# Kernel optimization log

Measured on AMD Instinct MI355X. Metric: run time of the kernel, lower is better.

The kernel has to match this reference:

```python
import jax, jax.numpy as jnp
import numpy as np

B, L, C = 8, 8192, 256
FOCAL_LEVEL = 3
KERNELS = [3, 5, 7]  # focal_factor*k + focal_x[0]
LN_EPS = 1e-3  # keras LayerNormalization default epsilon


def _gelu(x):
    return jax.nn.gelu(x, approximate=False)  # keras 'gelu' is exact


def _layernorm(x, g, b):
    m = jnp.mean(x, axis=-1, keepdims=True)
    v = jnp.var(x, axis=-1, keepdims=True)
    return (x - m) * jax.lax.rsqrt(v + LN_EPS) * g + b


def _conv1d_same(x, w, b):
    # x: [B,L,Cin], w: [K,Cin,Cout]
    y = jax.lax.conv_general_dilated(x, w, window_strides=(1,), padding='SAME',
                                     dimension_numbers=('NWC', 'WIO', 'NWC'))
    return y + b


def setup_inputs() -> dict:
    key = jax.random.key(0)
    ks = jax.random.split(key, 16)
    s = 0.02
    inp = {
        'x': jax.random.normal(ks[0], (B, L, C), dtype=jnp.float32),
        'f_w': jax.random.normal(ks[1], (C, 2 * C + FOCAL_LEVEL + 1), dtype=jnp.float32) * s,
        'f_b': jnp.zeros((2 * C + FOCAL_LEVEL + 1,), dtype=jnp.float32),
        'h_w': jax.random.normal(ks[2], (1, C, C), dtype=jnp.float32) * s,
        'h_b': jnp.zeros((C,), dtype=jnp.float32),
        'proj_w': jax.random.normal(ks[3], (C, C), dtype=jnp.float32) * s,
        'proj_b': jnp.zeros((C,), dtype=jnp.float32),
    }
    for l, K in enumerate(KERNELS):
        inp[f'conv_w{l}'] = jax.random.normal(ks[4 + l], (K, C, C), dtype=jnp.float32) * s
        inp[f'conv_b{l}'] = jnp.zeros((C,), dtype=jnp.float32)
        inp[f'ln_g{l}'] = jnp.ones((C,), dtype=jnp.float32)
        inp[f'ln_b{l}'] = jnp.zeros((C,), dtype=jnp.float32)
    return inp


def reference(x, f_w, f_b,
              conv_w0, conv_b0, ln_g0, ln_b0,
              conv_w1, conv_b1, ln_g1, ln_b1,
              conv_w2, conv_b2, ln_g2, ln_b2,
              h_w, h_b, proj_w, proj_b):
    x_fea = x @ f_w + f_b                      # [B,L,2C+4]
    q = x_fea[..., :C]
    ctx = x_fea[..., C:2 * C]
    gates = x_fea[..., 2 * C:]                 # [B,L,4]

    levels = [(conv_w0, conv_b0, ln_g0, ln_b0),
              (conv_w1, conv_b1, ln_g1, ln_b1),
              (conv_w2, conv_b2, ln_g2, ln_b2)]

    ctx_all = jnp.zeros_like(ctx)
    for l, (cw, cb, lg, lb) in enumerate(levels):
        ctx = _layernorm(_gelu(_conv1d_same(ctx, cw, cb)), lg, lb)
        ctx_all = ctx_all + ctx * gates[..., l:l + 1]

    # global average pool gate (broadcasts over L)
    ctx_global = jnp.mean(ctx, axis=1, keepdims=True) * gates[..., FOCAL_LEVEL:]
    ctx_all = ctx_all + ctx_global

    # h: 1x1 conv == dense
    ctx_all = jnp.einsum('blc,cd->bld', ctx_all, h_w[0]) + h_b
    x_out = (q * ctx_all) @ proj_w + proj_b    # proj_drop is identity at inference
    return x_out
```

## Files before the change

### kernel.cpp

```cpp
#include <hip/hip_runtime.h>
#include <math.h>

#define CDIM 256
#define LSEQ 8192
#define BATCH 8
#define MTOT (BATCH * LSEQ)
#define PADROWS 8208
#define PAD0 8

typedef unsigned short ushort_t;
typedef unsigned int uint_t;

typedef __bf16 bf16x8 __attribute__((ext_vector_type(8)));
typedef float f32x4 __attribute__((ext_vector_type(4)));

__device__ __forceinline__ ushort_t f2bf(float f) {
    union { float f; uint_t u; } v; v.f = f;
    uint_t u = v.u;
    return (ushort_t)((u + 0x7FFFu + ((u >> 16) & 1u)) >> 16);
}
__device__ __forceinline__ float bf2f(ushort_t h) {
    union { uint_t u; float f; } v; v.u = ((uint_t)h) << 16;
    return v.f;
}
__device__ __forceinline__ float gelu_exact(float x) {
    return 0.5f * x * (1.0f + erff(x * 0.70710678118654752440f));
}

__device__ __forceinline__ void gload16(const ushort_t* g, ushort_t* lds) {
    __builtin_amdgcn_global_load_lds(
        reinterpret_cast<__attribute__((address_space(1))) uint_t*>(
            reinterpret_cast<uintptr_t>(g)),
        reinterpret_cast<__attribute__((address_space(3))) uint_t*>(
            reinterpret_cast<uintptr_t>(lds)),
        16, 0, 0);
}

__global__ __launch_bounds__(256) void cvt_gates(
    const float* __restrict__ x, const float* __restrict__ f_w,
    const float* __restrict__ f_b,
    ushort_t* __restrict__ x_bf, float* __restrict__ gates)
{
    __shared__ float fcol[256][4];
    int tid = threadIdx.x;
    #pragma unroll
    for (int j = 0; j < 4; ++j) fcol[tid][j] = f_w[(size_t)tid * 516 + 512 + j];
    __syncthreads();
    int w = tid >> 6, l = tid & 63;
    size_t t = (size_t)blockIdx.x * 4 + w;
    float4 xv = ((const float4*)(x + t * CDIM))[l];
    ((ushort4*)(x_bf + t * CDIM))[l] =
        make_ushort4(f2bf(xv.x), f2bf(xv.y), f2bf(xv.z), f2bf(xv.w));
    int c = l * 4;
    float a[4];
    #pragma unroll
    for (int j = 0; j < 4; ++j)
        a[j] = xv.x * fcol[c][j] + xv.y * fcol[c + 1][j] + xv.z * fcol[c + 2][j] + xv.w * fcol[c + 3][j];
    #pragma unroll
    for (int off = 32; off >= 1; off >>= 1)
        #pragma unroll
        for (int j = 0; j < 4; ++j) a[j] += __shfl_xor(a[j], off);
    if (l == 0) {
        #pragma unroll
        for (int j = 0; j < 4; ++j) gates[t * 4 + j] = a[j] + f_b[512 + j];
    }
}

__global__ __launch_bounds__(256) void prep_weights(
    const float* __restrict__ f_w,  const float* __restrict__ c0,
    const float* __restrict__ c1,   const float* __restrict__ c2,
    const float* __restrict__ h_w,  const float* __restrict__ p_w,
    ushort_t* __restrict__ f_wT, ushort_t* __restrict__ c0T,
    ushort_t* __restrict__ c1T,  ushort_t* __restrict__ c2T,
    ushort_t* __restrict__ h_wT, ushort_t* __restrict__ p_wT)
{
    __shared__ float t[32][33];
    int r = blockIdx.x;
    const float* in; ushort_t* out; int Kt, ldin;
    if (r < 128)              { in = f_w; out = f_wT; Kt = 8;  ldin = 516; }
    else if ((r -= 128) < 192){ in = c0;  out = c0T;  Kt = 24; ldin = 256; }
    else if ((r -= 192) < 320){ in = c1;  out = c1T;  Kt = 40; ldin = 256; }
    else if ((r -= 320) < 448){ in = c2;  out = c2T;  Kt = 56; ldin = 256; }
    else if ((r -= 448) < 64) { in = h_w; out = h_wT; Kt = 8;  ldin = 256; }
    else                      { r -= 64; in = p_w; out = p_wT; Kt = 8; ldin = 256; }
    int K = Kt * 32;
    int k0 = (r % Kt) * 32, n0 = (r / Kt) * 32;
    int tx = threadIdx.x & 31, ty = threadIdx.x >> 5;
    #pragma unroll
    for (int i = 0; i < 4; i++) {
        int k = k0 + ty + i * 8;
        t[ty + i * 8][tx] = in[(size_t)k * ldin + n0 + tx];
    }
    __syncthreads();
    #pragma unroll
    for (int i = 0; i < 4; i++) {
        int n = n0 + ty + i * 8;
        out[(size_t)n * K + k0 + tx] = f2bf(t[tx][ty + i * 8]);
    }
}

__global__ __launch_bounds__(256) void zero_guards_all(ushort_t* __restrict__ ctx_base) {
    int i = blockIdx.x * 256 + threadIdx.x;
    int buf = i >> 15;
    int j = i & 32767;
    int c = j & 255;
    int rr = (j >> 8) & 15;
    int b = j >> 12;
    size_t row = (size_t)b * PADROWS + ((rr < 8) ? rr : (PADROWS - 16 + rr));
    ctx_base[((size_t)buf * BATCH * PADROWS + row) * CDIM + c] = 0;
}

__global__ __launch_bounds__(256) void fea_gemm(
    const ushort_t* __restrict__ A, const ushort_t* __restrict__ BT,
    const float* __restrict__ bias,
    ushort_t* __restrict__ q_out, ushort_t* __restrict__ ctx_pad)
{
    __shared__ __align__(16) ushort_t As[128 * 32];
    __shared__ __align__(16) ushort_t Bs[128 * 32];
    int tid = threadIdx.x;
    int w = tid >> 6, l = tid & 63;
    int bn = blockIdx.x * 128;
    int by = blockIdx.y;
    long arow0 = (long)by * 128;
    int crow0 = by * 128;

    int wr = w >> 1, wc = w & 1;
    int lr = l & 15, lk = (l >> 4) * 8;
    int sr = l >> 2;
    int sc = (l & 3) * 8;

    f32x4 acc[4][4] = {};

    for (int kt = 0; kt < 8; ++kt) {
        int k0 = kt << 5;
        #pragma unroll
        for (int jj = 0; jj < 2; ++jj) {
            int j = w * 2 + jj;
            int r = j * 16 + sr;
            gload16(A + (arow0 + r) * CDIM + (k0 + sc), &As[j * 512]);
            gload16(BT + (long)(bn + r) * 256 + (k0 + sc), &Bs[j * 512]);
        }
        __syncthreads();
        bf16x8 av[4], bv[4];
        #pragma unroll
        for (int m = 0; m < 4; ++m)
            av[m] = *reinterpret_cast<const bf16x8*>(&As[(wr * 64 + m * 16 + lr) * 32 + lk]);
        #pragma unroll
        for (int n = 0; n < 4; ++n)
            bv[n] = *reinterpret_cast<const bf16x8*>(&Bs[(wc * 64 + n * 16 + lr) * 32 + lk]);
        #pragma unroll
        for (int m = 0; m < 4; ++m)
            #pragma unroll
            for (int n = 0; n < 4; ++n)
                acc[m][n] = __builtin_amdgcn_mfma_f32_16x16x32_bf16(av[m], bv[n], acc[m][n], 0, 0, 0);
        __syncthreads();
    }

    int rbase = (l >> 4) * 4;
    #pragma unroll
    for (int n = 0; n < 4; ++n) {
        int col = bn + wc * 64 + n * 16 + lr;
        float bia = bias[col];
        #pragma unroll
        for (int m = 0; m < 4; ++m) {
            int rowb = crow0 + wr * 64 + m * 16 + rbase;
            #pragma unroll
            for (int r = 0; r < 4; ++r) {
                float v = acc[m][n][r] + bia;
                int row = rowb + r;
                if (col < CDIM) {
                    q_out[(size_t)row * CDIM + col] = f2bf(v);
                } else {
                    int bb = row >> 13, tb = row & (LSEQ - 1);
                    ctx_pad[((size_t)bb * PADROWS + PAD0 + tb) * CDIM + (col - CDIM)] = f2bf(v);
                }
            }
        }
    }
}

__device__ __forceinline__ void stageA128(const ushort_t* Arow0, int cc,
                                          ushort_t* asb, int tid, int w) {
    int row = tid >> 2, cp = tid & 3;
    int cg = cp ^ ((row >> 1) & 3);
    gload16(Arow0 + (size_t)row * CDIM + cc * 32 + cg * 8, asb + (size_t)(w * 64) * 8);
    if (tid < 64) {
        int o2 = 512 + tid;
        int row2 = o2 >> 2, cp2 = o2 & 3;
        int cg2 = cp2 ^ ((row2 >> 1) & 3);
        gload16(Arow0 + (size_t)row2 * CDIM + cc * 32 + cg2 * 8, asb + (size_t)512 * 8);
    }
}
__device__ __forceinline__ void stageB128(const ushort_t* BT, int Ktot, int koffB,
                                          ushort_t* bsb, int tid) {
    #pragma unroll
    for (int i = 0; i < 2; ++i) {
        int o = tid + i * 512;
        int n = o >> 2, cp = o & 3;
        int cg = cp ^ ((n >> 1) & 3);
        gload16(BT + (size_t)n * Ktot + koffB + cg * 8,
                bsb + (size_t)((o >> 6) * 64) * 8);
    }
}

__global__ __launch_bounds__(512, 4) void conv_fused(
    const ushort_t* __restrict__ A, const ushort_t* __restrict__ BT,
    const float* __restrict__ bias,
    const float* __restrict__ lng, const float* __restrict__ lnb,
    ushort_t* __restrict__ ctx_out, int KW, int Ktot)
{
    __shared__ __align__(16) ushort_t As2[2][144 * 32];
    __shared__ __align__(16) ushort_t Bs[2][256 * 32];

    int tid = threadIdx.x;
    int w = tid >> 6, l = tid & 63;
    int by = blockIdx.x;
    int b = by >> 6;
    int tloc = (by & 63) << 7;
    const ushort_t* Arow0 = A + ((size_t)b * PADROWS + PAD0 + tloc - 8) * CDIM;

    int wr = w >> 2;
    int wc = w & 3;
    int lr = l & 15;
    int quad = l >> 4;

    int P = KW >> 1;
    int hoff = 8 - P;
    f32x4 acc[4][4] = {};

    stageA128(Arow0, 0, As2[0], tid, w);
    stageB128(BT, Ktot, 0, Bs[0], tid);
    __syncthreads();

    int nIt = KW * 8;
    int it = 0;
    for (int c = 0; c < 8; ++c) {
        for (int tap = 0; tap < KW; ++tap, ++it) {
            if (tap == 0 && c < 7)
                stageA128(Arow0, c + 1, As2[(c + 1) & 1], tid, w);
            if (it + 1 < nIt) {
                int tapn = tap + 1, cn = c;
                if (tapn == KW) { tapn = 0; cn = c + 1; }
                stageB128(BT, Ktot, tapn * 256 + cn * 32, Bs[(it + 1) & 1], tid);
            }
            const ushort_t* asb = As2[c & 1];
            const ushort_t* bsb = Bs[it & 1];
            bf16x8 av[4], bv[4];
            #pragma unroll
            for (int m = 0; m < 4; ++m) {
                int row = wr * 64 + m * 16 + lr + tap + hoff;
                int cs = quad ^ ((row >> 1) & 3);
                av[m] = *reinterpret_cast<const bf16x8*>(&asb[row * 32 + cs * 8]);
            }
            #pragma unroll
            for (int n = 0; n < 4; ++n) {
                int nn = wc * 64 + n * 16 + lr;
                int cs = quad ^ ((nn >> 1) & 3);
                bv[n] = *reinterpret_cast<const bf16x8*>(&bsb[nn * 32 + cs * 8]);
            }
            #pragma unroll
            for (int m = 0; m < 4; ++m)
                #pragma unroll
                for (int n = 0; n < 4; ++n)
                    acc[m][n] = __builtin_amdgcn_mfma_f32_16x16x32_bf16(av[m], bv[n], acc[m][n], 0, 0, 0);
            __syncthreads();
        }
    }

    float* rs = (float*)&Bs[0][0];
    float* rq = rs + 512;
    float bias_c[4], lng_c[4], lnb_c[4];
    #pragma unroll
    for (int n = 0; n < 4; ++n) {
        int col = wc * 64 + n * 16 + lr;
        bias_c[n] = bias[col];
        lng_c[n] = lng[col];
        lnb_c[n] = lnb[col];
    }
    #pragma unroll
    for (int m = 0; m < 4; ++m) {
        #pragma unroll
        for (int r = 0; r < 4; ++r) {
            float s = 0.0f, sq = 0.0f;
            #pragma unroll
            for (int n = 0; n < 4; ++n) {
                float v = acc[m][n][r] + bias_c[n];
                v = gelu_exact(v);
                acc[m][n][r] = v;
                s += v; sq += v * v;
            }
            s += __shfl_xor(s, 1);  sq += __shfl_xor(sq, 1);
            s += __shfl_xor(s, 2);  sq += __shfl_xor(sq, 2);
            s += __shfl_xor(s, 4);  sq += __shfl_xor(sq, 4);
            s += __shfl_xor(s, 8);  sq += __shfl_xor(sq, 8);
            if (lr == 0) {
                int rl = wr * 64 + m * 16 + quad * 4 + r;
                rs[rl * 4 + wc] = s;
                rq[rl * 4 + wc] = sq;
            }
        }
    }
    __syncthreads();
    #pragma unroll
    for (int m = 0; m < 4; ++m) {
        #pragma unroll
        for (int r = 0; r < 4; ++r) {
            int rl = wr * 64 + m * 16 + quad * 4 + r;
            float mean = (rs[rl * 4] + rs[rl * 4 + 1] + rs[rl * 4 + 2] + rs[rl * 4 + 3]) * (1.0f / 256.0f);
            float var = (rq[rl * 4] + rq[rl * 4 + 1] + rq[rl * 4 + 2] + rq[rl * 4 + 3]) * (1.0f / 256.0f) - mean * mean;
            float inv = rsqrtf(var + 1e-3f);
            int trow = tloc + rl;
            ushort_t* cp = ctx_out + ((size_t)b * PADROWS + PAD0 + trow) * CDIM;
            #pragma unroll
            for (int n = 0; n < 4; ++n) {
                int col = wc * 64 + n * 16 + lr;
                float y = (acc[m][n][r] - mean) * inv * lng_c[n] + lnb_c[n];
                cp[col] = f2bf(y);
            }
        }
    }
}

__global__ __launch_bounds__(256) void col_mean_partial(const ushort_t* __restrict__ ctx_pad,
                                                        float* __restrict__ partial) {
    int b = blockIdx.x, chunk = blockIdx.y, c = threadIdx.x;
    const ushort_t* base = ctx_pad + ((size_t)b * PADROWS + PAD0 + chunk * 256) * CDIM + c;
    float s = 0.0f;
    for (int r = 0; r < 256; ++r) s += bf2f(base[(size_t)r * CDIM]);
    partial[((size_t)b * 32 + chunk) * CDIM + c] = s;
}

__global__ __launch_bounds__(256) void col_mean_final(const float* __restrict__ partial,
                                                      float* __restrict__ meanv) {
    int b = blockIdx.x, c = threadIdx.x;
    float s = 0.0f;
    for (int i = 0; i < 32; ++i) s += partial[((size_t)b * 32 + i) * CDIM + c];
    meanv[b * CDIM + c] = s * (1.0f / (float)LSEQ);
}

__global__ __launch_bounds__(512) void tail_fused(
    const ushort_t* __restrict__ ctx0, const ushort_t* __restrict__ ctx1,
    const ushort_t* __restrict__ ctx2,
    const float* __restrict__ gates, const float* __restrict__ meanv,
    const ushort_t* __restrict__ q_bf,
    const ushort_t* __restrict__ h_wT, const float* __restrict__ h_b,
    const ushort_t* __restrict__ proj_wT, const float* __restrict__ proj_b,
    float* __restrict__ out)
{
    __shared__ __align__(16) char pool[81920];
    ushort_t* As1 = (ushort_t*)pool;
    ushort_t* Bs1 = (ushort_t*)(pool + 8192);
    ushort_t* QC  = (ushort_t*)pool;
    ushort_t* Bs2 = (ushort_t*)(pool + 65536);

    int tid = threadIdx.x;
    int w = tid >> 6, l = tid & 63;
    long grow0 = (long)blockIdx.x * 128;

    int wr = w >> 2;
    int wc = w & 3;
    int lr = l & 15;
    int quad = l >> 4;
    int lk = quad * 8;

    int arow = tid >> 2;
    int seg = tid & 3;
    long grow_st = grow0 + arow;
    int b_st = (int)(grow_st >> 13), tb_st = (int)(grow_st & (LSEQ - 1));
    size_t prow = ((size_t)b_st * PADROWS + PAD0 + tb_st) * CDIM;
    float4 gv = *(const float4*)(gates + grow_st * 4);

    f32x4 acc[4][4] = {};

    for (int kt = 0; kt < 8; ++kt) {
        int col = kt * 32 + seg * 8;
        ushort4 a0 = *(const ushort4*)(ctx0 + prow + col);
        ushort4 a1 = *(const ushort4*)(ctx0 + prow + col + 4);
        ushort4 b0 = *(const ushort4*)(ctx1 + prow + col);
        ushort4 b1 = *(const ushort4*)(ctx1 + prow + col + 4);
        ushort4 d0 = *(const ushort4*)(ctx2 + prow + col);
        ushort4 d1 = *(const ushort4*)(ctx2 + prow + col + 4);
        float4 m0 = *(const float4*)(meanv + b_st * CDIM + col);
        float4 m1 = *(const float4*)(meanv + b_st * CDIM + col + 4);
        ushort_t va[8] = { a0.x, a0.y, a0.z, a0.w, a1.x, a1.y, a1.z, a1.w };
        ushort_t vb[8] = { b0.x, b0.y, b0.z, b0.w, b1.x, b1.y, b1.z, b1.w };
        ushort_t vd[8] = { d0.x, d0.y, d0.z, d0.w, d1.x, d1.y, d1.z, d1.w };
        float mv[8] = { m0.x, m0.y, m0.z, m0.w, m1.x, m1.y, m1.z, m1.w };
        ushort_t ov[8];
        #pragma unroll
        for (int j = 0; j < 8; ++j)
            ov[j] = f2bf(bf2f(va[j]) * gv.x + bf2f(vb[j]) * gv.y +
                         bf2f(vd[j]) * gv.z + mv[j] * gv.w);
        *(ushort4*)(As1 + arow * 32 + seg * 8)     = make_ushort4(ov[0], ov[1], ov[2], ov[3]);
        *(ushort4*)(As1 + arow * 32 + seg * 8 + 4) = make_ushort4(ov[4], ov[5], ov[6], ov[7]);
        #pragma unroll
        for (int i = 0; i < 2; ++i) {
            int o = tid + i * 512;
            int n = o >> 2, cp = o & 3;
            gload16(h_wT + (size_t)n * 256 + kt * 32 + cp * 8,
                    Bs1 + (size_t)((o >> 6) * 64) * 8);
        }
        __syncthreads();
        bf16x8 av[4], bv[4];
        #pragma unroll
        for (int m = 0; m < 4; ++m)
            av[m] = *reinterpret_cast<const bf16x8*>(&As1[(wr * 64 + m * 16 + lr) * 32 + lk]);
        #pragma unroll
        for (int n = 0; n < 4; ++n)
            bv[n] = *reinterpret_cast<const bf16x8*>(&Bs1[(wc * 64 + n * 16 + lr) * 32 + lk]);
        #pragma unroll
        for (int m = 0; m < 4; ++m)
            #pragma unroll
            for (int n = 0; n < 4; ++n)
                acc[m][n] = __builtin_amdgcn_mfma_f32_16x16x32_bf16(av[m], bv[n], acc[m][n], 0, 0, 0);
        __syncthreads();
    }

    {
        float hb_c[4];
        #pragma unroll
        for (int n = 0; n < 4; ++n) hb_c[n] = h_b[wc * 64 + n * 16 + lr];
        #pragma unroll
        for (int m = 0; m < 4; ++m) {
            #pragma unroll
            for (int r = 0; r < 4; ++r) {
                int row = wr * 64 + m * 16 + quad * 4 + r;
                long grow = grow0 + row;
                #pragma unroll
                for (int n = 0; n < 4; ++n) {
                    int col = wc * 64 + n * 16 + lr;
                    float v = acc[m][n][r] + hb_c[n];
                    float qv = bf2f(q_bf[(size_t)grow * CDIM + col]);
                    int c16 = (col >> 3) ^ (row & 7);
                    QC[row * 256 + c16 * 8 + (col & 7)] = f2bf(qv * v);
                }
            }
        }
    }
    __syncthreads();

    f32x4 acc2[4][4] = {};
    for (int kt = 0; kt < 8; ++kt) {
        #pragma unroll
        for (int i = 0; i < 2; ++i) {
            int o = tid + i * 512;
            int n = o >> 2, cp = o & 3;
            gload16(proj_wT + (size_t)n * 256 + kt * 32 + cp * 8,
                    Bs2 + (size_t)((o >> 6) * 64) * 8);
        }
        __syncthreads();
        bf16x8 av[4], bv[4];
        #pragma unroll
        for (int m = 0; m < 4; ++m) {
            int row = wr * 64 + m * 16 + lr;
            int c16 = (kt * 4 + quad) ^ (row & 7);
            av[m] = *reinterpret_cast<const bf16x8*>(&QC[row * 256 + c16 * 8]);
        }
        #pragma unroll
        for (int n = 0; n < 4; ++n)
            bv[n] = *reinterpret_cast<const bf16x8*>(&Bs2[(wc * 64 + n * 16 + lr) * 32 + lk]);
        #pragma unroll
        for (int m = 0; m < 4; ++m)
            #pragma unroll
            for (int n = 0; n < 4; ++n)
                acc2[m][n] = __builtin_amdgcn_mfma_f32_16x16x32_bf16(av[m], bv[n], acc2[m][n], 0, 0, 0);
        __syncthreads();
    }

    int rbase = quad * 4;
    #pragma unroll
    for (int n = 0; n < 4; ++n) {
        int col = wc * 64 + n * 16 + lr;
        float pb = proj_b[col];
        #pragma unroll
        for (int m = 0; m < 4; ++m) {
            #pragma unroll
            for (int r = 0; r < 4; ++r) {
                long grow = grow0 + wr * 64 + m * 16 + rbase + r;
                out[(size_t)grow * CDIM + col] = acc2[m][n][r] + pb;
            }
        }
    }
}

extern "C" void kernel_launch(void* const* d_in, const int* in_sizes, int n_in,
                              void* d_out, int out_size, void* d_ws, size_t ws_size,
                              hipStream_t stream) {
    const float* x      = (const float*)d_in[0];
    const float* f_w    = (const float*)d_in[1];
    const float* f_b    = (const float*)d_in[2];
    const float* h_w    = (const float*)d_in[3];
    const float* h_b    = (const float*)d_in[4];
    const float* proj_w = (const float*)d_in[5];
    const float* proj_b = (const float*)d_in[6];
    const float* conv_w[3] = { (const float*)d_in[7],  (const float*)d_in[11], (const float*)d_in[15] };
    const float* conv_b[3] = { (const float*)d_in[8],  (const float*)d_in[12], (const float*)d_in[16] };
    const float* ln_g[3]   = { (const float*)d_in[9],  (const float*)d_in[13], (const float*)d_in[17] };
    const float* ln_b[3]   = { (const float*)d_in[10], (const float*)d_in[14], (const float*)d_in[18] };

    const size_t MC = (size_t)MTOT * CDIM;
    const size_t PADC = (size_t)BATCH * PADROWS * CDIM;
    char* w = (char*)d_ws;
    ushort_t* x_bf  = (ushort_t*)w;  w += MC * 2;
    ushort_t* q_bf  = (ushort_t*)w;  w += MC * 2;
    ushort_t* ctxF  = (ushort_t*)w;  w += PADC * 2;
    ushort_t* ctx0  = (ushort_t*)w;  w += PADC * 2;
    ushort_t* ctx1  = (ushort_t*)w;  w += PADC * 2;
    ushort_t* ctx2  = (ushort_t*)w;  w += PADC * 2;
    float* gates    = (float*)w;     w += (size_t)MTOT * 4 * 4;
    float* partial  = (float*)w;     w += (size_t)8 * 32 * CDIM * 4;
    float* meanv    = (float*)w;     w += (size_t)8 * CDIM * 4;
    ushort_t* f_wT  = (ushort_t*)w;  w += (size_t)512 * 256 * 2;
    ushort_t* convT0 = (ushort_t*)w; w += (size_t)768 * 256 * 2;
    ushort_t* convT1 = (ushort_t*)w; w += (size_t)1280 * 256 * 2;
    ushort_t* convT2 = (ushort_t*)w; w += (size_t)1792 * 256 * 2;
    ushort_t* h_wT   = (ushort_t*)w; w += (size_t)256 * 256 * 2;
    ushort_t* proj_wT = (ushort_t*)w; w += (size_t)256 * 256 * 2;

    dim3 blk(256);

    cvt_gates<<<dim3(MTOT / 4), blk, 0, stream>>>(x, f_w, f_b, x_bf, gates);
    prep_weights<<<dim3(1216), blk, 0, stream>>>(f_w, conv_w[0], conv_w[1], conv_w[2],
        h_w, proj_w, f_wT, convT0, convT1, convT2, h_wT, proj_wT);
    zero_guards_all<<<dim3(512), blk, 0, stream>>>(ctxF);

    fea_gemm<<<dim3(4, 512), blk, 0, stream>>>(x_bf, f_wT, f_b, q_bf, ctxF);

    conv_fused<<<dim3(512), dim3(512), 0, stream>>>(ctxF, convT0, conv_b[0],
        ln_g[0], ln_b[0], ctx0, 3, 768);
    conv_fused<<<dim3(512), dim3(512), 0, stream>>>(ctx0, convT1, conv_b[1],
        ln_g[1], ln_b[1], ctx1, 5, 1280);
    conv_fused<<<dim3(512), dim3(512), 0, stream>>>(ctx1, convT2, conv_b[2],
        ln_g[2], ln_b[2], ctx2, 7, 1792);

    col_mean_partial<<<dim3(BATCH, 32), blk, 0, stream>>>(ctx2, partial);
    col_mean_final<<<dim3(BATCH), blk, 0, stream>>>(partial, meanv);

    tail_fused<<<dim3(512), dim3(512), 0, stream>>>(ctx0, ctx1, ctx2,
        gates, meanv, q_bf, h_wT, h_b, proj_wT, proj_b, (float*)d_out);
}
```

Baseline: 388.8 us.

## Split fused tail into separate combine+h GEMM and proj GEMM kernels

Replaces the single fused tail kernel, which kept the q*ctx intermediate in 80KB of shared memory, with two kernels using 256 threads and 128x128 tiles tiled over N. The gated combine and h projection write q*ctx as bf16 to global memory, reusing the x_bf buffer, and a separate GEMM applies proj. This aims for better occupancy and a smaller LDS footprint. The cost is an extra global round trip of the intermediate and recomputing the gated combine for each N tile.

```diff
diff --git a/kernel.cpp b/kernel.cpp
--- a/kernel.cpp
+++ b/kernel.cpp
@@ -338,34 +338,27 @@
     meanv[b * CDIM + c] = s * (1.0f / (float)LSEQ);
 }
 
-__global__ __launch_bounds__(512) void tail_fused(
+__global__ __launch_bounds__(256) void combine_h_gemm(
     const ushort_t* __restrict__ ctx0, const ushort_t* __restrict__ ctx1,
     const ushort_t* __restrict__ ctx2,
     const float* __restrict__ gates, const float* __restrict__ meanv,
     const ushort_t* __restrict__ q_bf,
     const ushort_t* __restrict__ h_wT, const float* __restrict__ h_b,
-    const ushort_t* __restrict__ proj_wT, const float* __restrict__ proj_b,
-    float* __restrict__ out)
+    ushort_t* __restrict__ qc_out)
 {
-    __shared__ __align__(16) char pool[81920];
-    ushort_t* As1 = (ushort_t*)pool;
-    ushort_t* Bs1 = (ushort_t*)(pool + 8192);
-    ushort_t* QC  = (ushort_t*)pool;
-    ushort_t* Bs2 = (ushort_t*)(pool + 65536);
-
+    __shared__ __align__(16) ushort_t As[128 * 32];
+    __shared__ __align__(16) ushort_t Bs[128 * 32];
     int tid = threadIdx.x;
     int w = tid >> 6, l = tid & 63;
-    long grow0 = (long)blockIdx.x * 128;
-
-    int wr = w >> 2;
-    int wc = w & 3;
-    int lr = l & 15;
-    int quad = l >> 4;
-    int lk = quad * 8;
-
-    int arow = tid >> 2;
-    int seg = tid & 3;
-    long grow_st = grow0 + arow;
+    int bn = blockIdx.x * 128;
+    long arow0 = (long)blockIdx.y * 128;
+
+    int wr = w >> 1, wc = w & 1;
+    int lr = l & 15, lk = (l >> 4) * 8;
+
+    int arow = tid >> 1;
+    int seg = tid & 1;
+    long grow_st = arow0 + arow;
     int b_st = (int)(grow_st >> 13), tb_st = (int)(grow_st & (LSEQ - 1));
     size_t prow = ((size_t)b_st * PADROWS + PAD0 + tb_st) * CDIM;
     float4 gv = *(const float4*)(gates + grow_st * 4);
@@ -373,41 +366,50 @@
     f32x4 acc[4][4] = {};
 
     for (int kt = 0; kt < 8; ++kt) {
-        int col = kt * 32 + seg * 8;
-        ushort4 a0 = *(const ushort4*)(ctx0 + prow + col);
-        ushort4 a1 = *(const ushort4*)(ctx0 + prow + col + 4);
-        ushort4 b0 = *(const ushort4*)(ctx1 + prow + col);
-        ushort4 b1 = *(const ushort4*)(ctx1 + prow + col + 4);
-        ushort4 d0 = *(const ushort4*)(ctx2 + prow + col);
-        ushort4 d1 = *(const ushort4*)(ctx2 + prow + col + 4);
-        float4 m0 = *(const float4*)(meanv + b_st * CDIM + col);
-        float4 m1 = *(const float4*)(meanv + b_st * CDIM + col + 4);
-        ushort_t va[8] = { a0.x, a0.y, a0.z, a0.w, a1.x, a1.y, a1.z, a1.w };
-        ushort_t vb[8] = { b0.x, b0.y, b0.z, b0.w, b1.x, b1.y, b1.z, b1.w };
-        ushort_t vd[8] = { d0.x, d0.y, d0.z, d0.w, d1.x, d1.y, d1.z, d1.w };
-        float mv[8] = { m0.x, m0.y, m0.z, m0.w, m1.x, m1.y, m1.z, m1.w };
-        ushort_t ov[8];
-        #pragma unroll
-        for (int j = 0; j < 8; ++j)
-            ov[j] = f2bf(bf2f(va[j]) * gv.x + bf2f(vb[j]) * gv.y +
-                         bf2f(vd[j]) * gv.z + mv[j] * gv.w);
-        *(ushort4*)(As1 + arow * 32 + seg * 8)     = make_ushort4(ov[0], ov[1], ov[2], ov[3]);
-        *(ushort4*)(As1 + arow * 32 + seg * 8 + 4) = make_ushort4(ov[4], ov[5], ov[6], ov[7]);
+        int col = kt * 32 + seg * 16;
+        ushort4 c0a = *(const ushort4*)(ctx0 + prow + col);
+        ushort4 c0b = *(const ushort4*)(ctx0 + prow + col + 4);
+        ushort4 c0c = *(const ushort4*)(ctx0 + prow + col + 8);
+        ushort4 c0d = *(const ushort4*)(ctx0 + prow + col + 12);
+        ushort4 c1a = *(const ushort4*)(ctx1 + prow + col);
+        ushort4 c1b = *(const ushort4*)(ctx1 + prow + col + 4);
+        ushort4 c1c = *(const ushort4*)(ctx1 + prow + col + 8);
+        ushort4 c1d = *(const ushort4*)(ctx1 + prow + col + 12);
+        ushort4 c2a = *(const ushort4*)(ctx2 + prow + col);
+        ushort4 c2b = *(const ushort4*)(ctx2 + prow + col + 4);
+        ushort4 c2c = *(const ushort4*)(ctx2 + prow + col + 8);
+        ushort4 c2d = *(const ushort4*)(ctx2 + prow + col + 12);
+        const float* mv = meanv + b_st * CDIM + col;
+        ushort_t v0[16] = { c0a.x,c0a.y,c0a.z,c0a.w, c0b.x,c0b.y,c0b.z,c0b.w,
+                            c0c.x,c0c.y,c0c.z,c0c.w, c0d.x,c0d.y,c0d.z,c0d.w };
+        ushort_t v1[16] = { c1a.x,c1a.y,c1a.z,c1a.w, c1b.x,c1b.y,c1b.z,c1b.w,
+                            c1c.x,c1c.y,c1c.z,c1c.w, c1d.x,c1d.y,c1d.z,c1d.w };
+        ushort_t v2[16] = { c2a.x,c2a.y,c2a.z,c2a.w, c2b.x,c2b.y,c2b.z,c2b.w,
+                            c2c.x,c2c.y,c2c.z,c2c.w, c2d.x,c2d.y,c2d.z,c2d.w };
+        ushort_t ov[16];
+        #pragma unroll
+        for (int j = 0; j < 16; ++j)
+            ov[j] = f2bf(bf2f(v0[j]) * gv.x + bf2f(v1[j]) * gv.y +
+                         bf2f(v2[j]) * gv.z + mv[j] * gv.w);
+        #pragma unroll
+        for (int j = 0; j < 4; ++j)
+            *(ushort4*)(&As[arow * 32 + seg * 16 + j * 4]) =
+                make_ushort4(ov[j*4], ov[j*4+1], ov[j*4+2], ov[j*4+3]);
         #pragma unroll
         for (int i = 0; i < 2; ++i) {
-            int o = tid + i * 512;
+            int o = tid + i * 256;
             int n = o >> 2, cp = o & 3;
-            gload16(h_wT + (size_t)n * 256 + kt * 32 + cp * 8,
-                    Bs1 + (size_t)((o >> 6) * 64) * 8);
+            gload16(h_wT + (size_t)(bn + n) * 256 + kt * 32 + cp * 8,
+                    &Bs[(size_t)(o & ~63) * 8]);
         }
         __syncthreads();
         bf16x8 av[4], bv[4];
         #pragma unroll
         for (int m = 0; m < 4; ++m)
-            av[m] = *reinterpret_cast<const bf16x8*>(&As1[(wr * 64 + m * 16 + lr) * 32 + lk]);
+            av[m] = *reinterpret_cast<const bf16x8*>(&As[(wr * 64 + m * 16 + lr) * 32 + lk]);
         #pragma unroll
         for (int n = 0; n < 4; ++n)
-            bv[n] = *reinterpret_cast<const bf16x8*>(&Bs1[(wc * 64 + n * 16 + lr) * 32 + lk]);
+            bv[n] = *reinterpret_cast<const bf16x8*>(&Bs[(wc * 64 + n * 16 + lr) * 32 + lk]);
         #pragma unroll
         for (int m = 0; m < 4; ++m)
             #pragma unroll
@@ -416,69 +418,79 @@
         __syncthreads();
     }
 
-    {
-        float hb_c[4];
-        #pragma unroll
-        for (int n = 0; n < 4; ++n) hb_c[n] = h_b[wc * 64 + n * 16 + lr];
+    int rbase = (l >> 4) * 4;
+    #pragma unroll
+    for (int n = 0; n < 4; ++n) {
+        int col = bn + wc * 64 + n * 16 + lr;
+        float hb = h_b[col];
         #pragma unroll
         for (int m = 0; m < 4; ++m) {
+            long rowb = arow0 + wr * 64 + m * 16 + rbase;
             #pragma unroll
             for (int r = 0; r < 4; ++r) {
-                int row = wr * 64 + m * 16 + quad * 4 + r;
-                long grow = grow0 + row;
-                #pragma unroll
-                for (int n = 0; n < 4; ++n) {
-                    int col = wc * 64 + n * 16 + lr;
-                    float v = acc[m][n][r] + hb_c[n];
-                    float qv = bf2f(q_bf[(size_t)grow * CDIM + col]);
-                    int c16 = (col >> 3) ^ (row & 7);
-                    QC[row * 256 + c16 * 8 + (col & 7)] = f2bf(qv * v);
-                }
-            }
-        }
-    }
-    __syncthreads();
-
-    f32x4 acc2[4][4] = {};
+                long row = rowb + r;
+                float v = acc[m][n][r] + hb;
+                float qv = bf2f(q_bf[(size_t)row * CDIM + col]);
+                qc_out[(size_t)row * CDIM + col] = f2bf(qv * v);
+            }
+        }
+    }
+}
+
+__global__ __launch_bounds__(256) void proj_gemm(
+    const ushort_t* __restrict__ A, const ushort_t* __restrict__ BT,
+    const float* __restrict__ bias, float* __restrict__ C)
+{
+    __shared__ __align__(16) ushort_t As[128 * 32];
+    __shared__ __align__(16) ushort_t Bs[128 * 32];
+    int tid = threadIdx.x;
+    int w = tid >> 6, l = tid & 63;
+    int bn = blockIdx.x * 128;
+    long arow0 = (long)blockIdx.y * 128;
+
+    int wr = w >> 1, wc = w & 1;
+    int lr = l & 15, lk = (l >> 4) * 8;
+    int sr = l >> 2;
+    int sc = (l & 3) * 8;
+
+    f32x4 acc[4][4] = {};
+
     for (int kt = 0; kt < 8; ++kt) {
-        #pragma unroll
-        for (int i = 0; i < 2; ++i) {
-            int o = tid + i * 512;
-            int n = o >> 2, cp = o & 3;
-            gload16(proj_wT + (size_t)n * 256 + kt * 32 + cp * 8,
-                    Bs2 + (size_t)((o >> 6) * 64) * 8);
+        int k0 = kt << 5;
+        #pragma unroll
+        for (int jj = 0; jj < 2; ++jj) {
+            int j = w * 2 + jj;
+            int r = j * 16 + sr;
+            gload16(A + (arow0 + r) * CDIM + (k0 + sc), &As[j * 512]);
+            gload16(BT + (long)(bn + r) * 256 + (k0 + sc), &Bs[j * 512]);
         }
         __syncthreads();
         bf16x8 av[4], bv[4];
         #pragma unroll
+        for (int m = 0; m < 4; ++m)
+            av[m] = *reinterpret_cast<const bf16x8*>(&As[(wr * 64 + m * 16 + lr) * 32 + lk]);
+        #pragma unroll
+        for (int n = 0; n < 4; ++n)
+            bv[n] = *reinterpret_cast<const bf16x8*>(&Bs[(wc * 64 + n * 16 + lr) * 32 + lk]);
+        #pragma unroll
+        for (int m = 0; m < 4; ++m)
+            #pragma unroll
+            for (int n = 0; n < 4; ++n)
+                acc[m][n] = __builtin_amdgcn_mfma_f32_16x16x32_bf16(av[m], bv[n], acc[m][n], 0, 0, 0);
+        __syncthreads();
+    }
+
+    int rbase = (l >> 4) * 4;
+    #pragma unroll
+    for (int n = 0; n < 4; ++n) {
+        int col = bn + wc * 64 + n * 16 + lr;
+        float bia = bias[col];
+        #pragma unroll
         for (int m = 0; m < 4; ++m) {
-            int row = wr * 64 + m * 16 + lr;
-            int c16 = (kt * 4 + quad) ^ (row & 7);
-            av[m] = *reinterpret_cast<const bf16x8*>(&QC[row * 256 + c16 * 8]);
-        }
-        #pragma unroll
-        for (int n = 0; n < 4; ++n)
-            bv[n] = *reinterpret_cast<const bf16x8*>(&Bs2[(wc * 64 + n * 16 + lr) * 32 + lk]);
-        #pragma unroll
-        for (int m = 0; m < 4; ++m)
-            #pragma unroll
-            for (int n = 0; n < 4; ++n)
-                acc2[m][n] = __builtin_amdgcn_mfma_f32_16x16x32_bf16(av[m], bv[n], acc2[m][n], 0, 0, 0);
-        __syncthreads();
-    }
-
-    int rbase = quad * 4;
-    #pragma unroll
-    for (int n = 0; n < 4; ++n) {
-        int col = wc * 64 + n * 16 + lr;
-        float pb = proj_b[col];
-        #pragma unroll
-        for (int m = 0; m < 4; ++m) {
-            #pragma unroll
-            for (int r = 0; r < 4; ++r) {
-                long grow = grow0 + wr * 64 + m * 16 + rbase + r;
-                out[(size_t)grow * CDIM + col] = acc2[m][n][r] + pb;
-            }
+            long rowb = arow0 + wr * 64 + m * 16 + rbase;
+            #pragma unroll
+            for (int r = 0; r < 4; ++r)
+                C[(size_t)(rowb + r) * CDIM + col] = acc[m][n][r] + bia;
         }
     }
 }
@@ -516,6 +528,7 @@
     ushort_t* convT2 = (ushort_t*)w; w += (size_t)1792 * 256 * 2;
     ushort_t* h_wT   = (ushort_t*)w; w += (size_t)256 * 256 * 2;
     ushort_t* proj_wT = (ushort_t*)w; w += (size_t)256 * 256 * 2;
+    ushort_t* qc_bf = x_bf;
 
     dim3 blk(256);
 
@@ -536,6 +549,9 @@
     col_mean_partial<<<dim3(BATCH, 32), blk, 0, stream>>>(ctx2, partial);
     col_mean_final<<<dim3(BATCH), blk, 0, stream>>>(partial, meanv);
 
-    tail_fused<<<dim3(512), dim3(512), 0, stream>>>(ctx0, ctx1, ctx2,
-        gates, meanv, q_bf, h_wT, h_b, proj_wT, proj_b, (float*)d_out);
-}
+    combine_h_gemm<<<dim3(2, 512), blk, 0, stream>>>(ctx0, ctx1, ctx2,
+        gates, meanv, q_bf, h_wT, h_b, qc_bf);
+
+    proj_gemm<<<dim3(2, 512), blk, 0, stream>>>(qc_bf, proj_wT, proj_b,
+        (float*)d_out);
+}
```

Result: faster. 380.4 us (-2.2%).
